# Optimization experiments

Hardware: AMD Instinct MI355X
Metric: run time of the kernel (lower is better)

The kernel has to match this reference:

```python
import jax, jax.numpy as jnp
import numpy as np

B, C = 2, 128
FMAP_HW = [(256, 256), (128, 128), (64, 64), (32, 32)]
N_ROIS = 4000
POOL = (7, 7)
N_ANCH = 300000
N_POS = 1000          # anchors with match > 0 (class 1)
N_NEG = 200000        # anchors with match == -1
SHEM_POOLSIZE = 20
N_CLASSES = 2


def setup_inputs() -> dict:
    key = jax.random.key(0)
    ks = jax.random.split(key, 10)
    inp = {}
    for l, (h, w) in enumerate(FMAP_HW):
        inp[f"fmap{l}"] = jax.random.normal(ks[l], (B, C, h, w), dtype=jnp.float32)
    # rois: normalized (y1, x1, y2, x2, batch_ix)
    ctr = jax.random.uniform(ks[4], (N_ROIS, 2))
    sz = jax.random.uniform(ks[5], (N_ROIS, 2), minval=0.02, maxval=0.5)
    lo = jnp.clip(ctr - sz / 2, 0.0, 1.0)
    hi = jnp.clip(ctr + sz / 2, 0.0, 1.0)
    bix = jax.random.randint(ks[6], (N_ROIS, 1), 0, B).astype(jnp.float32)
    inp["rois"] = jnp.concatenate([lo, hi, bix], axis=1)
    # fixed layout for static shapes: [pos | neg | neutral]
    am = np.zeros(N_ANCH, np.int32)
    am[:N_POS] = 1
    am[N_POS:N_POS + N_NEG] = -1
    inp["anchor_matches"] = jnp.asarray(am)
    inp["class_pred_logits"] = jax.random.normal(ks[7], (N_ANCH, N_CLASSES), dtype=jnp.float32)
    inp["pred_deltas"] = jax.random.normal(ks[8], (N_ANCH, 4), dtype=jnp.float32) * 0.1
    inp["target_deltas"] = jax.random.normal(ks[9], (N_ANCH, 4), dtype=jnp.float32) * 0.1
    return inp


def _roi_align_2d(fmap, boxes, batch_ix, pool):
    """Bilinear ROI align, one sample at each bin center.
    fmap: [B,C,H,W]; boxes: [N,4] in fmap pixel coords (y1,x1,y2,x2).
    Returns [N,C,ph,pw]."""
    Hc, Wc = fmap.shape[2], fmap.shape[3]
    ph, pw = pool
    y1, x1, y2, x2 = boxes[:, 0], boxes[:, 1], boxes[:, 2], boxes[:, 3]
    bh = (y2 - y1) / ph
    bw = (x2 - x1) / pw
    iy = jnp.arange(ph, dtype=jnp.float32) + 0.5
    ix = jnp.arange(pw, dtype=jnp.float32) + 0.5
    sy = jnp.clip(y1[:, None] + bh[:, None] * iy[None, :], 0.0, Hc - 1.0)  # [N,ph]
    sx = jnp.clip(x1[:, None] + bw[:, None] * ix[None, :], 0.0, Wc - 1.0)  # [N,pw]
    y0f = jnp.floor(sy)
    x0f = jnp.floor(sx)
    y0 = y0f.astype(jnp.int32)
    x0 = x0f.astype(jnp.int32)
    y1i = jnp.minimum(y0 + 1, Hc - 1)
    x1i = jnp.minimum(x0 + 1, Wc - 1)
    wy = (sy - y0f)[:, :, None, None]  # [N,ph,1,1]
    wx = (sx - x0f)[:, None, :, None]  # [N,1,pw,1]
    b = batch_ix[:, None, None]

    def gather(yy, xx):
        # yy [N,ph], xx [N,pw] -> [N,ph,pw,C]
        return fmap[b, :, yy[:, :, None], xx[:, None, :]]

    v00 = gather(y0, x0)
    v01 = gather(y0, x1i)
    v10 = gather(y1i, x0)
    v11 = gather(y1i, x1i)
    out = (v00 * (1 - wy) * (1 - wx) + v01 * (1 - wy) * wx
           + v10 * wy * (1 - wx) + v11 * wy * wx)
    return jnp.transpose(out, (0, 3, 1, 2))


def _forward(fmaps, rois, anchor_matches, class_pred_logits, pred_deltas, target_deltas):
    boxes = rois[:, :4]
    batch_ix = rois[:, 4].astype(jnp.int32)
    h = boxes[:, 2] - boxes[:, 0]
    w = boxes[:, 3] - boxes[:, 1]
    roi_level = jnp.clip(
        jnp.round(4.0 + jnp.log2(jnp.sqrt(h * w + 1e-12))).astype(jnp.int32), 0, 3)
    boxes_sg = jax.lax.stop_gradient(boxes)  # original detaches level_boxes
    pooled = jnp.zeros((N_ROIS, C, POOL[0], POOL[1]), fmaps[0].dtype)
    for lvl, f in enumerate(fmaps):
        He, We = f.shape[2], f.shape[3]
        lb = boxes_sg * jnp.array([He, We, He, We], jnp.float32)
        pl = _roi_align_2d(f, lb, batch_ix, POOL)
        mask = (roi_level == lvl).astype(pl.dtype)[:, None, None, None]
        pooled = pooled + mask * pl  # each roi hits exactly one level; order preserved

    # ---- class loss with SHEM (layout: [:N_POS] pos, [N_POS:N_POS+N_NEG] neg) ----
    pos_logits = class_pred_logits[:N_POS]
    pos_targets = anchor_matches[:N_POS].astype(jnp.int32)
    pos_logp = jax.nn.log_softmax(pos_logits, axis=1)
    pos_loss = -jnp.mean(jnp.take_along_axis(pos_logp, pos_targets[:, None], axis=1))

    neg_logits = class_pred_logits[N_POS:N_POS + N_NEG]
    neg_bg_prob = jax.nn.softmax(neg_logits, axis=1)[:, 0]
    negative_count = N_POS  # max(1, n_pos)
    pool_n = min(negative_count * SHEM_POOLSIZE, N_NEG)
    order = jnp.argsort(neg_bg_prob)          # ascending bg prob = hardest first
    pool_idx = order[:pool_n]
    perm = jax.random.permutation(jax.random.key(1), pool_n)
    neg_ix = pool_idx[perm[:negative_count]]  # stochastic draw from hard pool
    neg_loss = -jnp.mean(jax.nn.log_softmax(neg_logits[neg_ix], axis=1)[:, 0])
    class_loss = (pos_loss + neg_loss) / 2.0

    # ---- bbox smooth-L1 on positives (beta=1, mean reduction) ----
    diff = jnp.abs(pred_deltas[:N_POS] - target_deltas[:N_POS])
    sl1 = jnp.where(diff < 1.0, 0.5 * diff * diff, diff - 0.5)
    bbox_loss = jnp.mean(sl1)
    return pooled, class_loss, bbox_loss


def reference(fmap0, fmap1, fmap2, fmap3, rois, anchor_matches,
              class_pred_logits, pred_deltas, target_deltas):
    return _forward([fmap0, fmap1, fmap2, fmap3], rois, anchor_matches,
                    class_pred_logits, pred_deltas, target_deltas)
```

## Files before the change

kernel.cpp:

```cpp
#include <hip/hip_runtime.h>
#include <hip/hip_bf16.h>
#include <cstdint>

#define NROIS  4000
#define NCH    128
#define NBINS  49
#define N_POSA 1000
#define N_NEGA 200000
#define POOLN  20000
#define HBITS_A 13
#define ABINS  8192
#define PBINS  4096
#define SUBN   4096
#define NTRBLK 2720
#define NPREP  106
#define NRANKA 512
#define NRANKP 40
#define TPAD   136

#define L0OFF 0ull
#define L1OFF 16777216ull
#define L2OFF 20971520ull
#define L3OFF 22020096ull
#define TLELEMS 22282240ull

__device__ __forceinline__ uint32_t rotl32d(uint32_t v, int r) { return (v << r) | (v >> (32-r)); }

__device__ void tf2x32(uint32_t k0, uint32_t k1, uint32_t& x0, uint32_t& x1)
{
    const uint32_t ks2 = k0 ^ k1 ^ 0x1BD11BDAu;
    const int R0[4] = {13,15,26,6};
    const int R1[4] = {17,29,16,24};
    x0 += k0; x1 += k1;
#pragma unroll
    for (int r = 0; r < 4; ++r) { x0 += x1; x1 = rotl32d(x1, R0[r]); x1 ^= x0; }
    x0 += k1;  x1 += ks2 + 1u;
#pragma unroll
    for (int r = 0; r < 4; ++r) { x0 += x1; x1 = rotl32d(x1, R1[r]); x1 ^= x0; }
    x0 += ks2; x1 += k0 + 2u;
#pragma unroll
    for (int r = 0; r < 4; ++r) { x0 += x1; x1 = rotl32d(x1, R0[r]); x1 ^= x0; }
    x0 += k0;  x1 += k1 + 3u;
#pragma unroll
    for (int r = 0; r < 4; ++r) { x0 += x1; x1 = rotl32d(x1, R1[r]); x1 ^= x0; }
    x0 += k1;  x1 += ks2 + 4u;
#pragma unroll
    for (int r = 0; r < 4; ++r) { x0 += x1; x1 = rotl32d(x1, R0[r]); x1 ^= x0; }
    x0 += ks2; x1 += k0 + 5u;
}

__device__ __forceinline__ unsigned int monobits(float x) {
    unsigned int u = __float_as_uint(x);
    return (u & 0x80000000u) ? ~u : (u | 0x80000000u);
}

__device__ __forceinline__ unsigned short f2bf(float x) {
    union { __hip_bfloat16 h; unsigned short u; } c;
    c.h = __float2bfloat16(x);
    return c.u;
}

__global__ void k_zero(unsigned int* __restrict__ h)
{
    h[blockIdx.x*256 + threadIdx.x] = 0u;
}

__global__ __launch_bounds__(256) void k_trprep(
    const float* __restrict__ f0, const float* __restrict__ f1,
    const float* __restrict__ f2, const float* __restrict__ f3,
    __hip_bfloat16* __restrict__ tl,
    unsigned long long* __restrict__ T1, unsigned long long* __restrict__ T2,
    unsigned int* __restrict__ histA,
    unsigned int* __restrict__ histP1, unsigned int* __restrict__ histP2,
    const int* __restrict__ am, const float* __restrict__ logits,
    const float* __restrict__ pd, const float* __restrict__ td,
    float* __restrict__ prt, int ntr)
{
    __shared__ __align__(16) unsigned char smraw[32768];
    const int bid = blockIdx.x;
    const int t   = threadIdx.x;

    if (bid < ntr) {
        unsigned short* s = (unsigned short*)smraw;
        const int bz = bid / 1360;
        const int r  = bid - bz*1360;
        int lvl, tile;
        if      (r < 1024) { lvl = 0; tile = r; }
        else if (r < 1280) { lvl = 1; tile = r - 1024; }
        else if (r < 1344) { lvl = 2; tile = r - 1280; }
        else               { lvl = 3; tile = r - 1344; }
        const int HW = 65536 >> (2*lvl);
        const float* in = (lvl==0) ? f0 : (lvl==1) ? f1 : (lvl==2) ? f2 : f3;
        const size_t ooff = (lvl==0) ? L0OFF : (lvl==1) ? L1OFF : (lvl==2) ? L2OFF : L3OFF;
        const int hw0 = tile * 64;
        const float4* in4 = (const float4*)(in + (size_t)bz * 128 * HW);
        const int HW4 = HW >> 2;
        const int h4b = hw0 >> 2;
#pragma unroll
        for (int k = 0; k < 8; ++k) {
            const int idx = t + k*256;
            const int c   = idx >> 4;
            const int h4  = idx & 15;
            const float4 v = in4[(size_t)c * HW4 + h4b + h4];
            const int r0 = h4 * 4;
            const int cs = c ^ ((h4 & 7) << 3);
            s[(r0+0)*TPAD + cs] = f2bf(v.x);
            s[(r0+1)*TPAD + cs] = f2bf(v.y);
            s[(r0+2)*TPAD + cs] = f2bf(v.z);
            s[(r0+3)*TPAD + cs] = f2bf(v.w);
        }
        __syncthreads();
        uint4* out4 = (uint4*)(tl + ooff + (size_t)bz * (size_t)HW * 128
                                         + (size_t)hw0 * 128);
        const int rr = t >> 4;
        const int q  = t & 15;
        const int c8 = q * 8;
#pragma unroll
        for (int m = 0; m < 4; ++m) {
            const int row = rr + m*16;
            const int sw = ((row >> 2) & 7) << 3;
            out4[row*16 + q] = *(const uint4*)&s[row*TPAD + (c8 ^ sw)];
        }
        return;
    }

    const int pbid = bid - ntr;
    if (pbid < 40) {
        unsigned int* buf = (unsigned int*)smraw;
        unsigned int* lh1 = buf;
        unsigned int* lh2 = buf + PBINS;
        for (int b = t; b < 2*PBINS; b += 256) buf[b] = 0u;
        __syncthreads();
        const int i = pbid*256 + t;
        if (i < POOLN/2) {
            uint32_t a0 = 0u, a1 = 2u; tf2x32(0u, 1u, a0, a1);
            uint32_t b0 = 1u, b1 = 3u; tf2x32(0u, 1u, b0, b1);
            uint32_t c0 = 0u, c1 = 2u; tf2x32(a0, b0, c0, c1);
            uint32_t d0 = 1u, d1 = 3u; tf2x32(a0, b0, d0, d1);
            uint32_t x0 = (uint32_t)i, x1 = (uint32_t)(POOLN/2 + i);
            tf2x32(a1, b1, x0, x1);
            T1[i]           = ((unsigned long long)x0 << 32) | (unsigned)i;
            T1[POOLN/2 + i] = ((unsigned long long)x1 << 32) | (unsigned)(POOLN/2 + i);
            atomicAdd(&lh1[x0 >> 20], 1u);
            atomicAdd(&lh1[x1 >> 20], 1u);
            uint32_t y0 = (uint32_t)i, y1 = (uint32_t)(POOLN/2 + i);
            tf2x32(c1, d1, y0, y1);
            T2[i]           = ((unsigned long long)y0 << 32) | (unsigned)i;
            T2[POOLN/2 + i] = ((unsigned long long)y1 << 32) | (unsigned)(POOLN/2 + i);
            atomicAdd(&lh2[y0 >> 20], 1u);
            atomicAdd(&lh2[y1 >> 20], 1u);
        }
        __syncthreads();
        for (int b = t; b < PBINS; b += 256) {
            unsigned int v = lh1[b]; if (v) atomicAdd(&histP1[b], v);
            v = lh2[b];              if (v) atomicAdd(&histP2[b], v);
        }
        return;
    }
    if (pbid < 104) {
        unsigned int* buf = (unsigned int*)smraw;
        for (int b = t; b < ABINS; b += 256) buf[b] = 0u;
        __syncthreads();
        for (int i = (pbid-40)*256 + t; i < N_NEGA; i += 64*256) {
            const float l0 = logits[(size_t)(N_POSA+i)*2+0];
            const float l1 = logits[(size_t)(N_POSA+i)*2+1];
            atomicAdd(&buf[monobits(l0 - l1) >> (32-HBITS_A)], 1u);
        }
        __syncthreads();
        for (int b = t; b < ABINS; b += 256) {
            const unsigned int v = buf[b];
            if (v) atomicAdd(&histA[b], v);
        }
        return;
    }
    float* red = (float*)smraw;
    float s = 0.0f;
    if (pbid == 104) {
        for (int i = t; i < N_POSA; i += 256) {
            const int tgt = am[i];
            const float l0 = logits[(size_t)i*2+0], l1 = logits[(size_t)i*2+1];
            const float m = fmaxf(l0, l1);
            const float lse = logf(expf(l0-m) + expf(l1-m));
            const float lt = (tgt == 0) ? l0 : l1;
            s += (lt - m) - lse;
        }
    } else {
        for (int i = t; i < N_POSA*4; i += 256) {
            const float d = fabsf(pd[i] - td[i]);
            s += (d < 1.0f) ? 0.5f*d*d : d - 0.5f;
        }
    }
    red[t] = s;
    __syncthreads();
    for (int off = 128; off > 0; off >>= 1) {
        if (t < off) red[t] += red[t+off];
        __syncthreads();
    }
    if (t == 0) prt[pbid - 104] = red[0];
}

__device__ void scan_one256(const unsigned int* __restrict__ hist,
                            unsigned int* __restrict__ base,
                            unsigned int* __restrict__ basem,
                            int n, unsigned int* lds)
{
    const int t = threadIdx.x;
    const int chunk = n >> 8;
    unsigned int s = 0;
    for (int k = 0; k < chunk; ++k) s += hist[t*chunk + k];
    lds[t] = s;
    __syncthreads();
    for (int off = 1; off < 256; off <<= 1) {
        unsigned int v = (t >= off) ? lds[t-off] : 0u;
        __syncthreads();
        lds[t] += v;
        __syncthreads();
    }
    unsigned int run = (t == 0) ? 0u : lds[t-1];
    for (int k = 0; k < chunk; ++k) {
        base[t*chunk+k] = run; basem[t*chunk+k] = run;
        run += hist[t*chunk+k];
    }
    if (t == 255) { base[n] = run; basem[n] = run; }
    __syncthreads();
}

__device__ void scan_all(const unsigned int* histA, const unsigned int* histP1,
                         const unsigned int* histP2,
                         unsigned int* baseA,  unsigned int* baseAm,
                         unsigned int* baseP1, unsigned int* baseP1m,
                         unsigned int* baseP2, unsigned int* baseP2m,
                         unsigned int* sel, unsigned int* lds)
{
    scan_one256(histA, baseA, baseAm, ABINS, lds);
    scan_one256(histP1, baseP1, baseP1m, PBINS, lds);
    scan_one256(histP2, baseP2, baseP2m, PBINS, lds);
    const int t = threadIdx.x;
    const int chunk = ABINS >> 8;
    for (int k = 0; k < chunk; ++k) {
        const int bin = t*chunk + k;
        if (baseA[bin] < POOLN && baseA[bin] + histA[bin] >= POOLN)
            sel[0] = (unsigned int)bin;
    }
}

__global__ __launch_bounds__(256) void k_roiscan(
    const __hip_bfloat16* __restrict__ tl, const float* __restrict__ rois,
    float* __restrict__ out,
    const unsigned int* __restrict__ histA,
    const unsigned int* __restrict__ histP1, const unsigned int* __restrict__ histP2,
    unsigned int* __restrict__ baseA,  unsigned int* __restrict__ baseAm,
    unsigned int* __restrict__ baseP1, unsigned int* __restrict__ baseP1m,
    unsigned int* __restrict__ baseP2, unsigned int* __restrict__ baseP2m,
    unsigned int* __restrict__ sel, int nroi)
{
    __shared__ int   s_a[NBINS][4];
    __shared__ float s_w[NBINS][4];
    __shared__ float s_o[NCH * NBINS];
    const int n   = blockIdx.x;
    const int tid = threadIdx.x;

    if (n >= nroi) {
        scan_all(histA, histP1, histP2, baseA, baseAm, baseP1, baseP1m,
                 baseP2, baseP2m, sel, (unsigned int*)s_o);
        return;
    }

    const float ry1 = rois[n*5+0], rx1 = rois[n*5+1];
    const float ry2 = rois[n*5+2], rx2 = rois[n*5+3];
    const int   b   = (int)rois[n*5+4];
    const float h = ry2 - ry1, w = rx2 - rx1;
    const float lraw = rintf(4.0f + log2f(sqrtf(h*w + 1e-12f)));
    int lvl = (int)lraw; lvl = lvl < 0 ? 0 : (lvl > 3 ? 3 : lvl);
    const int H = 256 >> lvl;
    const size_t lbase = (lvl==0) ? L0OFF : (lvl==1) ? L1OFF : (lvl==2) ? L2OFF : L3OFF;
    const __hip_bfloat16* bp = tl + lbase + (size_t)b * (size_t)(H*H) * NCH;

    const float Hf  = (float)H;
    const float y1p = ry1*Hf, x1p = rx1*Hf, y2p = ry2*Hf, x2p = rx2*Hf;
    const float bh = (y2p - y1p) / 7.0f, bw = (x2p - x1p) / 7.0f;

    if (tid < NBINS) {
        const int py = tid / 7, px = tid % 7;
        float sy = y1p + bh*((float)py + 0.5f);
        float sx = x1p + bw*((float)px + 0.5f);
        sy = fminf(fmaxf(sy, 0.0f), Hf - 1.0f);
        sx = fminf(fmaxf(sx, 0.0f), Hf - 1.0f);
        const float y0f = floorf(sy), x0f = floorf(sx);
        const int y0 = (int)y0f, x0 = (int)x0f;
        const int y1i = min(y0+1, H-1), x1i = min(x0+1, H-1);
        const float wy = sy - y0f, wx = sx - x0f;
        s_a[tid][0] = y0 *H + x0;
        s_a[tid][1] = y0 *H + x1i;
        s_a[tid][2] = y1i*H + x0;
        s_a[tid][3] = y1i*H + x1i;
        const float omy = 1.0f - wy, omx = 1.0f - wx;
        s_w[tid][0] = omy*omx; s_w[tid][1] = omy*wx;
        s_w[tid][2] = wy *omx; s_w[tid][3] = wy *wx;
    }
    __syncthreads();

    const int c4 = tid & 31;
    const int bg = tid >> 5;
    for (int bin = bg; bin < NBINS; bin += 8) {
        float a0 = 0.f, a1 = 0.f, a2 = 0.f, a3 = 0.f;
#pragma unroll
        for (int tap = 0; tap < 4; ++tap) {
            const uint2 v = *(const uint2*)(bp + (size_t)s_a[bin][tap] * NCH + 4*c4);
            const float wgt = s_w[bin][tap];
            a0 += __uint_as_float(v.x << 16)         * wgt;
            a1 += __uint_as_float(v.x & 0xffff0000u) * wgt;
            a2 += __uint_as_float(v.y << 16)         * wgt;
            a3 += __uint_as_float(v.y & 0xffff0000u) * wgt;
        }
        s_o[(4*c4+0)*NBINS + bin] = a0;
        s_o[(4*c4+1)*NBINS + bin] = a1;
        s_o[(4*c4+2)*NBINS + bin] = a2;
        s_o[(4*c4+3)*NBINS + bin] = a3;
    }
    __syncthreads();

    float4* outn = (float4*)(out + (size_t)n * (NCH*NBINS));
    const float4* so4 = (const float4*)s_o;
    for (int t4 = tid; t4 < (NCH*NBINS)/4; t4 += 256)
        outn[t4] = so4[t4];
}

__global__ __launch_bounds__(256) void k_roi(
    const float* __restrict__ f0, const float* __restrict__ f1,
    const float* __restrict__ f2, const float* __restrict__ f3,
    const float* __restrict__ rois, float* __restrict__ out)
{
    __shared__ int   s_a[NBINS][4];
    __shared__ float s_w[NBINS][4];
    const int n   = blockIdx.x;
    const int tid = threadIdx.x;

    const float ry1 = rois[n*5+0], rx1 = rois[n*5+1];
    const float ry2 = rois[n*5+2], rx2 = rois[n*5+3];
    const int   b   = (int)rois[n*5+4];
    const float h = ry2 - ry1, w = rx2 - rx1;
    const float lraw = rintf(4.0f + log2f(sqrtf(h*w + 1e-12f)));
    int lvl = (int)lraw; lvl = lvl < 0 ? 0 : (lvl > 3 ? 3 : lvl);
    const int H = 256 >> lvl;
    const float* f = (lvl==0) ? f0 : (lvl==1) ? f1 : (lvl==2) ? f2 : f3;

    const float Hf  = (float)H;
    const float y1p = ry1*Hf, x1p = rx1*Hf, y2p = ry2*Hf, x2p = rx2*Hf;
    const float bh = (y2p - y1p) / 7.0f, bw = (x2p - x1p) / 7.0f;

    if (tid < NBINS) {
        const int py = tid / 7, px = tid % 7;
        float sy = y1p + bh*((float)py + 0.5f);
        float sx = x1p + bw*((float)px + 0.5f);
        sy = fminf(fmaxf(sy, 0.0f), Hf - 1.0f);
        sx = fminf(fmaxf(sx, 0.0f), Hf - 1.0f);
        const float y0f = floorf(sy), x0f = floorf(sx);
        const int y0 = (int)y0f, x0 = (int)x0f;
        const int y1i = min(y0+1, H-1), x1i = min(x0+1, H-1);
        const float wy = sy - y0f, wx = sx - x0f;
        s_a[tid][0] = y0 *H + x0;
        s_a[tid][1] = y0 *H + x1i;
        s_a[tid][2] = y1i*H + x0;
        s_a[tid][3] = y1i*H + x1i;
        const float omy = 1.0f - wy, omx = 1.0f - wx;
        s_w[tid][0] = omy*omx; s_w[tid][1] = omy*wx;
        s_w[tid][2] = wy *omx; s_w[tid][3] = wy *wx;
    }
    __syncthreads();

    const int hw = H*H;
    const float* basep = f + (size_t)b * NCH * hw;
    float* outn = out + (size_t)n * (NCH*NBINS);
    for (int t = tid; t < NCH*NBINS; t += 256) {
        const int c   = t / NBINS;
        const int bin = t - c*NBINS;
        const float* p = basep + (size_t)c * hw;
        outn[t] = p[s_a[bin][0]]*s_w[bin][0] + p[s_a[bin][1]]*s_w[bin][1]
                + p[s_a[bin][2]]*s_w[bin][2] + p[s_a[bin][3]]*s_w[bin][3];
    }
}

__global__ __launch_bounds__(256) void k_scatter(
    const float* __restrict__ logits,
    const unsigned long long* __restrict__ T1, const unsigned long long* __restrict__ T2,
    unsigned long long* __restrict__ A,
    unsigned long long* __restrict__ P1, unsigned long long* __restrict__ P2,
    unsigned int* __restrict__ baseAm, unsigned int* __restrict__ baseP1m,
    unsigned int* __restrict__ baseP2m, const unsigned int* __restrict__ sel)
{
    __shared__ unsigned int lh[ABINS];
    const int bid = blockIdx.x;
    const int t   = threadIdx.x;
    if (bid < 64) {
        for (int b = t; b < ABINS; b += 256) lh[b] = 0u;
        __syncthreads();
        const unsigned int selv = sel[0];
        const int start = bid * (N_NEGA/64);
        const int end   = start + (N_NEGA/64);
        for (int i = start + t; i < end; i += 256) {
            const float l0 = logits[(size_t)(N_POSA+i)*2+0];
            const float l1 = logits[(size_t)(N_POSA+i)*2+1];
            const unsigned int bin = monobits(l0 - l1) >> (32-HBITS_A);
            if (bin <= selv) atomicAdd(&lh[bin], 1u);
        }
        __syncthreads();
        for (int b = t; b < ABINS; b += 256) {
            const unsigned int cnt = lh[b];
            if (cnt) lh[b] = atomicAdd(&baseAm[b], cnt);
        }
        __syncthreads();
        for (int i = start + t; i < end; i += 256) {
            const float l0 = logits[(size_t)(N_POSA+i)*2+0];
            const float l1 = logits[(size_t)(N_POSA+i)*2+1];
            const unsigned int bits = monobits(l0 - l1);
            const unsigned int bin = bits >> (32-HBITS_A);
            if (bin <= selv) {
                const unsigned int pos = atomicAdd(&lh[bin], 1u);
                A[pos] = ((unsigned long long)bits << 32) | (unsigned)i;
            }
        }
        return;
    }
    const int i = (bid - 64)*256 + t;
    if (i < POOLN) {
        const unsigned long long k1 = T1[i];
        const unsigned int p1 = atomicAdd(&baseP1m[(unsigned)(k1 >> 52)], 1u);
        P1[p1] = k1;
        const unsigned long long k2 = T2[i];
        const unsigned int p2 = atomicAdd(&baseP2m[(unsigned)(k2 >> 52)], 1u);
        P2[p2] = k2;
    }
}

__global__ __launch_bounds__(1024) void k_rank(
    const unsigned long long* __restrict__ A,
    const unsigned long long* __restrict__ P1, const unsigned long long* __restrict__ P2,
    const unsigned int* __restrict__ baseA,
    const unsigned int* __restrict__ baseP1, const unsigned int* __restrict__ baseP2,
    const unsigned int* __restrict__ sel,
    unsigned int* __restrict__ As, unsigned int* __restrict__ P1s,
    unsigned int* __restrict__ P2s)
{
    __shared__ unsigned long long g[SUBN];
    __shared__ unsigned int h2[SUBN];
    __shared__ unsigned int h2b[SUBN];
    const int bid = blockIdx.x;
    const int t   = threadIdx.x;
    if (bid < NRANKA) {
        const unsigned int selv = sel[0];
        for (unsigned int bin = (unsigned)bid; bin <= selv; bin += NRANKA) {
            const int base = (int)baseA[bin];
            const int cnt  = (int)baseA[bin+1] - base;
            if (cnt <= 0) continue;
            if (cnt == 1) {
                if (t == 0) As[base] = (unsigned)(A[base] & 0xffffffffu);
                continue;
            }
            if (cnt <= SUBN) {
                for (int b = t; b < SUBN; b += 1024) h2[b] = 0u;
                __syncthreads();
                for (int k = t; k < cnt; k += 1024) {
                    const unsigned int sub = ((unsigned)(A[base+k] >> 32) >> 7) & (SUBN-1);
                    atomicAdd(&h2[sub], 1u);
                }
                __syncthreads();
                unsigned int c0 = h2[4*t+0], c1 = h2[4*t+1],
                             c2 = h2[4*t+2], c3 = h2[4*t+3];
                h2b[t] = c0 + c1 + c2 + c3;
                __syncthreads();
                for (int off = 1; off < 1024; off <<= 1) {
                    const unsigned int v = (t >= off) ? h2b[t-off] : 0u;
                    __syncthreads();
                    h2b[t] += v;
                    __syncthreads();
                }
                unsigned int run = (t == 0) ? 0u : h2b[t-1];
                __syncthreads();
                h2[4*t+0] = run; h2b[4*t+0] = run; run += c0;
                h2[4*t+1] = run; h2b[4*t+1] = run; run += c1;
                h2[4*t+2] = run; h2b[4*t+2] = run; run += c2;
                h2[4*t+3] = run; h2b[4*t+3] = run; run += c3;
                __syncthreads();
                for (int k = t; k < cnt; k += 1024) {
                    const unsigned long long key = A[base+k];
                    const unsigned int sub = ((unsigned)(key >> 32) >> 7) & (SUBN-1);
                    const unsigned int p = atomicAdd(&h2[sub], 1u);
                    g[p] = key;
                }
                __syncthreads();
                for (int p = t; p < cnt; p += 1024) {
                    const unsigned long long key = g[p];
                    const unsigned int sub = ((unsigned)(key >> 32) >> 7) & (SUBN-1);
                    const int b0 = (int)h2b[sub], e0 = (int)h2[sub];
                    int r = b0;
                    for (int q = b0; q < e0; ++q) r += (g[q] < key) ? 1 : 0;
                    As[base + r] = (unsigned)(key & 0xffffffffu);
                }
                __syncthreads();
            } else {
                for (int k = t; k < cnt; k += 1024) {
                    const unsigned long long key = A[base+k];
                    int rank = 0;
                    for (int j = 0; j < cnt; ++j) rank += (A[base+j] < key) ? 1 : 0;
                    As[base + rank] = (unsigned)(key & 0xffffffffu);
                }
            }
        }
        return;
    }
    const int gg = (bid - NRANKA)*1024 + t;
    if (gg < POOLN) {
        const unsigned long long key = P1[gg];
        const unsigned int bin = (unsigned)(key >> 52);
        const int b0 = (int)baseP1[bin], b1 = (int)baseP1[bin+1];
        int rank = 0;
        for (int j = b0; j < b1; ++j) rank += (P1[j] < key) ? 1 : 0;
        P1s[b0 + rank] = (unsigned)(key & 0xffffffffu);
    } else if (gg < 2*POOLN) {
        const int e = gg - POOLN;
        const unsigned long long key = P2[e];
        const unsigned int bin = (unsigned)(key >> 52);
        const int b0 = (int)baseP2[bin], b1 = (int)baseP2[bin+1];
        int rank = 0;
        for (int j = b0; j < b1; ++j) rank += (P2[j] < key) ? 1 : 0;
        P2s[b0 + rank] = (unsigned)(key & 0xffffffffu);
    }
}

__global__ __launch_bounds__(256) void k_final(
    const float* __restrict__ logits, const unsigned int* __restrict__ As,
    const unsigned int* __restrict__ P1s, const unsigned int* __restrict__ P2s,
    const float* __restrict__ partial, float* __restrict__ out2)
{
    __shared__ float red[256];
    const int t = threadIdx.x;
    float s = 0.0f;
    for (int j = t; j < N_POSA; j += 256) {
        const unsigned int i2 = P2s[j];
        const unsigned int r  = P1s[i2];
        const unsigned int i  = As[r];
        const float l0 = logits[(size_t)(N_POSA+i)*2+0];
        const float l1 = logits[(size_t)(N_POSA+i)*2+1];
        const float m = fmaxf(l0, l1);
        s += (l0 - m) - logf(expf(l0-m) + expf(l1-m));
    }
    red[t] = s;
    __syncthreads();
    for (int off = 128; off > 0; off >>= 1) {
        if (t < off) red[t] += red[t+off];
        __syncthreads();
    }
    if (t == 0) {
        const float neg_loss = -red[0] / (float)N_POSA;
        const float pos_loss = -partial[0] / (float)N_POSA;
        out2[0] = 0.5f * (pos_loss + neg_loss);
        out2[1] = partial[1] / (float)(N_POSA*4);
    }
}

extern "C" void kernel_launch(void* const* d_in, const int* in_sizes, int n_in,
                              void* d_out, int out_size, void* d_ws, size_t ws_size,
                              hipStream_t stream)
{
    const float* f0     = (const float*)d_in[0];
    const float* f1     = (const float*)d_in[1];
    const float* f2     = (const float*)d_in[2];
    const float* f3     = (const float*)d_in[3];
    const float* rois   = (const float*)d_in[4];
    const int*   am     = (const int*)  d_in[5];
    const float* logits = (const float*)d_in[6];
    const float* pd     = (const float*)d_in[7];
    const float* td     = (const float*)d_in[8];
    float* out = (float*)d_out;

    char* ws = (char*)d_ws;
    unsigned long long* A      = (unsigned long long*)(ws);
    unsigned long long* T1     = (unsigned long long*)(ws +  262144);
    unsigned long long* T2     = (unsigned long long*)(ws +  422144);
    unsigned long long* P1     = (unsigned long long*)(ws +  582144);
    unsigned long long* P2     = (unsigned long long*)(ws +  742144);
    unsigned int*       histA  = (unsigned int*)      (ws +  902144);
    unsigned int*       histP1 = (unsigned int*)      (ws +  934912);
    unsigned int*       histP2 = (unsigned int*)      (ws +  951296);
    unsigned int*       baseA  = (unsigned int*)      (ws +  967680);
    unsigned int*       baseAm = (unsigned int*)      (ws + 1000512);
    unsigned int*       baseP1 = (unsigned int*)      (ws + 1033344);
    unsigned int*       baseP1m= (unsigned int*)      (ws + 1049792);
    unsigned int*       baseP2 = (unsigned int*)      (ws + 1066240);
    unsigned int*       baseP2m= (unsigned int*)      (ws + 1082688);
    unsigned int*       sel    = (unsigned int*)      (ws + 1099136);
    float*              prt    = (float*)             (ws + 1099200);
    __hip_bfloat16*     tl     = (__hip_bfloat16*)    (ws + 1099264);
    unsigned int*       As     = (unsigned int*)T1;
    unsigned int*       P1s    = (unsigned int*)T2;
    unsigned int*       P2s    = (unsigned int*)((char*)T2 + 80000);
    const size_t NEED = 1099264ull + TLELEMS * 2ull;
    const bool use_cl = (ws_size >= NEED);

    k_zero<<<64, 256, 0, stream>>>(histA);

    if (use_cl) {
        k_trprep<<<NTRBLK + NPREP, 256, 0, stream>>>(f0, f1, f2, f3, tl,
                                                     T1, T2, histA, histP1, histP2,
                                                     am, logits, pd, td, prt, NTRBLK);
        k_roiscan<<<NROIS + 1, 256, 0, stream>>>(tl, rois, out,
                                                 histA, histP1, histP2,
                                                 baseA, baseAm, baseP1, baseP1m,
                                                 baseP2, baseP2m, sel, NROIS);
    } else {
        k_trprep<<<NPREP, 256, 0, stream>>>(f0, f1, f2, f3, tl,
                                            T1, T2, histA, histP1, histP2,
                                            am, logits, pd, td, prt, 0);
        k_roi<<<NROIS, 256, 0, stream>>>(f0, f1, f2, f3, rois, out);
        k_roiscan<<<1, 256, 0, stream>>>(tl, rois, out,
                                         histA, histP1, histP2,
                                         baseA, baseAm, baseP1, baseP1m,
                                         baseP2, baseP2m, sel, 0);
    }

    k_scatter<<<64 + (POOLN+255)/256, 256, 0, stream>>>(logits, T1, T2, A, P1, P2,
                                                        baseAm, baseP1m, baseP2m, sel);

    k_rank<<<NRANKA + NRANKP, 1024, 0, stream>>>(A, P1, P2, baseA, baseP1, baseP2,
                                                 sel, As, P1s, P2s);

    k_final<<<1, 256, 0, stream>>>(logits, As, P1s, P2s, prt,
                                   out + (size_t)NROIS*NCH*NBINS);
}
```

Measured before the change: 102.8 us.

## Interleave transpose and ROI-align blocks with the sort stages across launches

```diff
diff --git a/kernel.cpp b/kernel.cpp
--- a/kernel.cpp
+++ b/kernel.cpp
@@ -12,10 +12,11 @@
 #define ABINS  8192
 #define PBINS  4096
 #define SUBN   4096
-#define NTRBLK 2720
+#define NTR_H  1360
 #define NPREP  106
+#define NSCAT  143
 #define NRANKA 512
-#define NRANKP 40
+#define NRANKP 157
 #define TPAD   136
 
 #define L0OFF 0ull
@@ -65,7 +66,124 @@
     h[blockIdx.x*256 + threadIdx.x] = 0u;
 }
 
-__global__ __launch_bounds__(256) void k_trprep(
+__device__ void do_transpose(int trid, const float* __restrict__ f0,
+                             const float* __restrict__ f1, const float* __restrict__ f2,
+                             const float* __restrict__ f3,
+                             __hip_bfloat16* __restrict__ tl, unsigned char* smraw)
+{
+    unsigned short* s = (unsigned short*)smraw;
+    const int t  = threadIdx.x;
+    const int bz = trid / NTR_H;
+    const int r  = trid - bz*NTR_H;
+    int lvl, tile;
+    if      (r < 1024) { lvl = 0; tile = r; }
+    else if (r < 1280) { lvl = 1; tile = r - 1024; }
+    else if (r < 1344) { lvl = 2; tile = r - 1280; }
+    else               { lvl = 3; tile = r - 1344; }
+    const int HW = 65536 >> (2*lvl);
+    const float* in = (lvl==0) ? f0 : (lvl==1) ? f1 : (lvl==2) ? f2 : f3;
+    const size_t ooff = (lvl==0) ? L0OFF : (lvl==1) ? L1OFF : (lvl==2) ? L2OFF : L3OFF;
+    const int hw0 = tile * 64;
+    const float4* in4 = (const float4*)(in + (size_t)bz * 128 * HW);
+    const int HW4 = HW >> 2;
+    const int h4b = hw0 >> 2;
+#pragma unroll
+    for (int k = 0; k < 8; ++k) {
+        const int idx = t + k*256;
+        const int c   = idx >> 4;
+        const int h4  = idx & 15;
+        const float4 v = in4[(size_t)c * HW4 + h4b + h4];
+        const int r0 = h4 * 4;
+        const int cs = c ^ ((h4 & 7) << 3);
+        s[(r0+0)*TPAD + cs] = f2bf(v.x);
+        s[(r0+1)*TPAD + cs] = f2bf(v.y);
+        s[(r0+2)*TPAD + cs] = f2bf(v.z);
+        s[(r0+3)*TPAD + cs] = f2bf(v.w);
+    }
+    __syncthreads();
+    uint4* out4 = (uint4*)(tl + ooff + (size_t)bz * (size_t)HW * 128
+                                     + (size_t)hw0 * 128);
+    const int rr = t >> 4;
+    const int q  = t & 15;
+    const int c8 = q * 8;
+#pragma unroll
+    for (int m = 0; m < 4; ++m) {
+        const int row = rr + m*16;
+        const int sw = ((row >> 2) & 7) << 3;
+        out4[row*16 + q] = *(const uint4*)&s[row*TPAD + (c8 ^ sw)];
+    }
+}
+
+__device__ void do_roi(int n, const __hip_bfloat16* __restrict__ tl,
+                       const float* __restrict__ rois, float* __restrict__ out,
+                       unsigned char* smraw)
+{
+    int   (*s_a)[4] = (int(*)[4])smraw;
+    float (*s_w)[4] = (float(*)[4])(smraw + 784);
+    float* s_o      = (float*)(smraw + 1568);
+    const int tid = threadIdx.x;
+
+    const float ry1 = rois[n*5+0], rx1 = rois[n*5+1];
+    const float ry2 = rois[n*5+2], rx2 = rois[n*5+3];
+    const int   b   = (int)rois[n*5+4];
+    const float h = ry2 - ry1, w = rx2 - rx1;
+    const float lraw = rintf(4.0f + log2f(sqrtf(h*w + 1e-12f)));
+    int lvl = (int)lraw; lvl = lvl < 0 ? 0 : (lvl > 3 ? 3 : lvl);
+    const int H = 256 >> lvl;
+    const size_t lbase = (lvl==0) ? L0OFF : (lvl==1) ? L1OFF : (lvl==2) ? L2OFF : L3OFF;
+    const __hip_bfloat16* bp = tl + lbase + (size_t)b * (size_t)(H*H) * NCH;
+
+    const float Hf  = (float)H;
+    const float y1p = ry1*Hf, x1p = rx1*Hf, y2p = ry2*Hf, x2p = rx2*Hf;
+    const float bh = (y2p - y1p) / 7.0f, bw = (x2p - x1p) / 7.0f;
+
+    if (tid < NBINS) {
+        const int py = tid / 7, px = tid % 7;
+        float sy = y1p + bh*((float)py + 0.5f);
+        float sx = x1p + bw*((float)px + 0.5f);
+        sy = fminf(fmaxf(sy, 0.0f), Hf - 1.0f);
+        sx = fminf(fmaxf(sx, 0.0f), Hf - 1.0f);
+        const float y0f = floorf(sy), x0f = floorf(sx);
+        const int y0 = (int)y0f, x0 = (int)x0f;
+        const int y1i = min(y0+1, H-1), x1i = min(x0+1, H-1);
+        const float wy = sy - y0f, wx = sx - x0f;
+        s_a[tid][0] = y0 *H + x0;
+        s_a[tid][1] = y0 *H + x1i;
+        s_a[tid][2] = y1i*H + x0;
+        s_a[tid][3] = y1i*H + x1i;
+        const float omy = 1.0f - wy, omx = 1.0f - wx;
+        s_w[tid][0] = omy*omx; s_w[tid][1] = omy*wx;
+        s_w[tid][2] = wy *omx; s_w[tid][3] = wy *wx;
+    }
+    __syncthreads();
+
+    const int c4 = tid & 31;
+    const int bg = tid >> 5;
+    for (int bin = bg; bin < NBINS; bin += 8) {
+        float a0 = 0.f, a1 = 0.f, a2 = 0.f, a3 = 0.f;
+#pragma unroll
+        for (int tap = 0; tap < 4; ++tap) {
+            const uint2 v = *(const uint2*)(bp + (size_t)s_a[bin][tap] * NCH + 4*c4);
+            const float wgt = s_w[bin][tap];
+            a0 += __uint_as_float(v.x << 16)         * wgt;
+            a1 += __uint_as_float(v.x & 0xffff0000u) * wgt;
+            a2 += __uint_as_float(v.y << 16)         * wgt;
+            a3 += __uint_as_float(v.y & 0xffff0000u) * wgt;
+        }
+        s_o[(4*c4+0)*NBINS + bin] = a0;
+        s_o[(4*c4+1)*NBINS + bin] = a1;
+        s_o[(4*c4+2)*NBINS + bin] = a2;
+        s_o[(4*c4+3)*NBINS + bin] = a3;
+    }
+    __syncthreads();
+
+    float4* outn = (float4*)(out + (size_t)n * (NCH*NBINS));
+    const float4* so4 = (const float4*)s_o;
+    for (int t4 = tid; t4 < (NCH*NBINS)/4; t4 += 256)
+        outn[t4] = so4[t4];
+}
+
+__global__ __launch_bounds__(256) void k_stage1(
     const float* __restrict__ f0, const float* __restrict__ f1,
     const float* __restrict__ f2, const float* __restrict__ f3,
     __hip_bfloat16* __restrict__ tl,
@@ -80,49 +198,7 @@
     const int bid = blockIdx.x;
     const int t   = threadIdx.x;
 
-    if (bid < ntr) {
-        unsigned short* s = (unsigned short*)smraw;
-        const int bz = bid / 1360;
-        const int r  = bid - bz*1360;
-        int lvl, tile;
-        if      (r < 1024) { lvl = 0; tile = r; }
-        else if (r < 1280) { lvl = 1; tile = r - 1024; }
-        else if (r < 1344) { lvl = 2; tile = r - 1280; }
-        else               { lvl = 3; tile = r - 1344; }
-        const int HW = 65536 >> (2*lvl);
-        const float* in = (lvl==0) ? f0 : (lvl==1) ? f1 : (lvl==2) ? f2 : f3;
-        const size_t ooff = (lvl==0) ? L0OFF : (lvl==1) ? L1OFF : (lvl==2) ? L2OFF : L3OFF;
-        const int hw0 = tile * 64;
-        const float4* in4 = (const float4*)(in + (size_t)bz * 128 * HW);
-        const int HW4 = HW >> 2;
-        const int h4b = hw0 >> 2;
-#pragma unroll
-        for (int k = 0; k < 8; ++k) {
-            const int idx = t + k*256;
-            const int c   = idx >> 4;
-            const int h4  = idx & 15;
-            const float4 v = in4[(size_t)c * HW4 + h4b + h4];
-            const int r0 = h4 * 4;
-            const int cs = c ^ ((h4 & 7) << 3);
-            s[(r0+0)*TPAD + cs] = f2bf(v.x);
-            s[(r0+1)*TPAD + cs] = f2bf(v.y);
-            s[(r0+2)*TPAD + cs] = f2bf(v.z);
-            s[(r0+3)*TPAD + cs] = f2bf(v.w);
-        }
-        __syncthreads();
-        uint4* out4 = (uint4*)(tl + ooff + (size_t)bz * (size_t)HW * 128
-                                         + (size_t)hw0 * 128);
-        const int rr = t >> 4;
-        const int q  = t & 15;
-        const int c8 = q * 8;
-#pragma unroll
-        for (int m = 0; m < 4; ++m) {
-            const int row = rr + m*16;
-            const int sw = ((row >> 2) & 7) << 3;
-            out4[row*16 + q] = *(const uint4*)&s[row*TPAD + (c8 ^ sw)];
-        }
-        return;
-    }
+    if (bid < ntr) { do_transpose(bid, f0, f1, f2, f3, tl, smraw); return; }
 
     const int pbid = bid - ntr;
     if (pbid < 40) {
@@ -225,13 +301,22 @@
     __syncthreads();
 }
 
-__device__ void scan_all(const unsigned int* histA, const unsigned int* histP1,
-                         const unsigned int* histP2,
-                         unsigned int* baseA,  unsigned int* baseAm,
-                         unsigned int* baseP1, unsigned int* baseP1m,
-                         unsigned int* baseP2, unsigned int* baseP2m,
-                         unsigned int* sel, unsigned int* lds)
-{
+__global__ __launch_bounds__(256) void k_stage2(
+    const float* __restrict__ f0, const float* __restrict__ f1,
+    const float* __restrict__ f2, const float* __restrict__ f3,
+    __hip_bfloat16* __restrict__ tl,
+    const unsigned int* __restrict__ histA,
+    const unsigned int* __restrict__ histP1, const unsigned int* __restrict__ histP2,
+    unsigned int* __restrict__ baseA,  unsigned int* __restrict__ baseAm,
+    unsigned int* __restrict__ baseP1, unsigned int* __restrict__ baseP1m,
+    unsigned int* __restrict__ baseP2, unsigned int* __restrict__ baseP2m,
+    unsigned int* __restrict__ sel, int ntr)
+{
+    __shared__ __align__(16) unsigned char smraw[32768];
+    const int bid = blockIdx.x;
+    if (bid < ntr) { do_transpose(bid + NTR_H, f0, f1, f2, f3, tl, smraw); return; }
+
+    unsigned int* lds = (unsigned int*)smraw;
     scan_one256(histA, baseA, baseAm, ABINS, lds);
     scan_one256(histP1, baseP1, baseP1m, PBINS, lds);
     scan_one256(histP2, baseP2, baseP2m, PBINS, lds);
@@ -244,27 +329,188 @@
     }
 }
 
-__global__ __launch_bounds__(256) void k_roiscan(
+__global__ __launch_bounds__(256) void k_stage3(
+    const __hip_bfloat16* __restrict__ tl, const float* __restrict__ rois,
+    float* __restrict__ out, const float* __restrict__ logits,
+    const unsigned long long* __restrict__ T1, const unsigned long long* __restrict__ T2,
+    unsigned long long* __restrict__ A,
+    unsigned long long* __restrict__ P1, unsigned long long* __restrict__ P2,
+    unsigned int* __restrict__ baseAm, unsigned int* __restrict__ baseP1m,
+    unsigned int* __restrict__ baseP2m, const unsigned int* __restrict__ sel,
+    int rcnt)
+{
+    __shared__ __align__(16) unsigned char smraw[32768];
+    const int bid = blockIdx.x;
+    const int t   = threadIdx.x;
+    if (bid < rcnt) { do_roi(bid, tl, rois, out, smraw); return; }
+
+    const int sbid = bid - rcnt;
+    if (sbid < 64) {
+        unsigned int* lh = (unsigned int*)smraw;
+        for (int b = t; b < ABINS; b += 256) lh[b] = 0u;
+        __syncthreads();
+        const unsigned int selv = sel[0];
+        const int start = sbid * (N_NEGA/64);
+        const int end   = start + (N_NEGA/64);
+        for (int i = start + t; i < end; i += 256) {
+            const float l0 = logits[(size_t)(N_POSA+i)*2+0];
+            const float l1 = logits[(size_t)(N_POSA+i)*2+1];
+            const unsigned int bin = monobits(l0 - l1) >> (32-HBITS_A);
+            if (bin <= selv) atomicAdd(&lh[bin], 1u);
+        }
+        __syncthreads();
+        for (int b = t; b < ABINS; b += 256) {
+            const unsigned int cnt = lh[b];
+            if (cnt) lh[b] = atomicAdd(&baseAm[b], cnt);
+        }
+        __syncthreads();
+        for (int i = start + t; i < end; i += 256) {
+            const float l0 = logits[(size_t)(N_POSA+i)*2+0];
+            const float l1 = logits[(size_t)(N_POSA+i)*2+1];
+            const unsigned int bits = monobits(l0 - l1);
+            const unsigned int bin = bits >> (32-HBITS_A);
+            if (bin <= selv) {
+                const unsigned int pos = atomicAdd(&lh[bin], 1u);
+                A[pos] = ((unsigned long long)bits << 32) | (unsigned)i;
+            }
+        }
+        return;
+    }
+    const int i = (sbid - 64)*256 + t;
+    if (i < POOLN) {
+        const unsigned long long k1 = T1[i];
+        const unsigned int p1 = atomicAdd(&baseP1m[(unsigned)(k1 >> 52)], 1u);
+        P1[p1] = k1;
+        const unsigned long long k2 = T2[i];
+        const unsigned int p2 = atomicAdd(&baseP2m[(unsigned)(k2 >> 52)], 1u);
+        P2[p2] = k2;
+    }
+}
+
+__global__ __launch_bounds__(256) void k_stage4(
     const __hip_bfloat16* __restrict__ tl, const float* __restrict__ rois,
     float* __restrict__ out,
-    const unsigned int* __restrict__ histA,
-    const unsigned int* __restrict__ histP1, const unsigned int* __restrict__ histP2,
-    unsigned int* __restrict__ baseA,  unsigned int* __restrict__ baseAm,
-    unsigned int* __restrict__ baseP1, unsigned int* __restrict__ baseP1m,
-    unsigned int* __restrict__ baseP2, unsigned int* __restrict__ baseP2m,
-    unsigned int* __restrict__ sel, int nroi)
+    const unsigned long long* __restrict__ A,
+    const unsigned long long* __restrict__ P1, const unsigned long long* __restrict__ P2,
+    const unsigned int* __restrict__ baseA,
+    const unsigned int* __restrict__ baseP1, const unsigned int* __restrict__ baseP2,
+    const unsigned int* __restrict__ sel,
+    unsigned int* __restrict__ As, unsigned int* __restrict__ P1s,
+    unsigned int* __restrict__ P2s, int rcnt)
+{
+    __shared__ __align__(16) unsigned char smraw[32768];
+    const int bid = blockIdx.x;
+    const int t   = threadIdx.x;
+    if (bid < rcnt) { do_roi(2000 + bid, tl, rois, out, smraw); return; }
+
+    const int sbid = bid - rcnt;
+    if (sbid < NRANKA) {
+        unsigned int*   gkey = (unsigned int*)smraw;
+        unsigned short* gsub = (unsigned short*)(smraw + 16384);
+        unsigned int*   h2p  = (unsigned int*)(smraw + 24576);
+        unsigned int*   st   = (unsigned int*)(smraw + 16384);
+        const unsigned int selv = sel[0];
+        for (unsigned int bin = (unsigned)sbid; bin <= selv; bin += NRANKA) {
+            const int base = (int)baseA[bin];
+            const int cnt  = (int)baseA[bin+1] - base;
+            if (cnt <= 0) continue;
+            if (cnt == 1) {
+                if (t == 0) As[base] = (unsigned)(A[base] & 0xffffffffu);
+                continue;
+            }
+            if (cnt <= SUBN) {
+                for (int b = t; b < SUBN/2; b += 256) h2p[b] = 0u;
+                __syncthreads();
+                for (int k = t; k < cnt; k += 256) {
+                    const unsigned int sub =
+                        ((unsigned)(A[base+k] >> 32) >> 7) & (SUBN-1);
+                    atomicAdd(&h2p[sub >> 1], 1u << ((sub & 1) << 4));
+                }
+                __syncthreads();
+                unsigned int tmp[8];
+                unsigned int s = 0;
+                for (int w = 0; w < 8; ++w) {
+                    const unsigned int v = h2p[t*8 + w];
+                    tmp[w] = v;
+                    s += (v & 0xFFFFu) + (v >> 16);
+                }
+                st[t] = s;
+                __syncthreads();
+                for (int off = 1; off < 256; off <<= 1) {
+                    const unsigned int v = (t >= off) ? st[t-off] : 0u;
+                    __syncthreads();
+                    st[t] += v;
+                    __syncthreads();
+                }
+                unsigned int run = (t == 0) ? 0u : st[t-1];
+                __syncthreads();
+                for (int w = 0; w < 8; ++w) {
+                    const unsigned int v = tmp[w];
+                    const unsigned int lo = run; run += (v & 0xFFFFu);
+                    const unsigned int hi = run; run += (v >> 16);
+                    h2p[t*8 + w] = lo | (hi << 16);
+                }
+                __syncthreads();
+                for (int k = t; k < cnt; k += 256) {
+                    const unsigned long long key = A[base+k];
+                    const unsigned int bits = (unsigned)(key >> 32);
+                    const unsigned int sub  = (bits >> 7) & (SUBN-1);
+                    const unsigned int sh   = (sub & 1) << 4;
+                    const unsigned int old  = atomicAdd(&h2p[sub >> 1], 1u << sh);
+                    const unsigned int pos  = (old >> sh) & 0xFFFFu;
+                    gkey[pos] = ((bits & 0x7Fu) << 18) | (unsigned)(key & 0xffffffffu);
+                    gsub[pos] = (unsigned short)sub;
+                }
+                __syncthreads();
+                for (int p = t; p < cnt; p += 256) {
+                    const unsigned int k25 = gkey[p];
+                    const unsigned short sb = gsub[p];
+                    int b0 = p; while (b0 > 0 && gsub[b0-1] == sb) --b0;
+                    int e0 = p; while (e0+1 < cnt && gsub[e0+1] == sb) ++e0;
+                    int r = b0;
+                    for (int q = b0; q <= e0; ++q) r += (gkey[q] < k25) ? 1 : 0;
+                    As[base + r] = k25 & 0x3FFFFu;
+                }
+                __syncthreads();
+            } else {
+                for (int k = t; k < cnt; k += 256) {
+                    const unsigned long long key = A[base+k];
+                    int rank = 0;
+                    for (int j = 0; j < cnt; ++j) rank += (A[base+j] < key) ? 1 : 0;
+                    As[base + rank] = (unsigned)(key & 0xffffffffu);
+                }
+            }
+        }
+        return;
+    }
+    const int g = (sbid - NRANKA)*256 + t;
+    if (g < POOLN) {
+        const unsigned long long key = P1[g];
+        const unsigned int bin = (unsigned)(key >> 52);
+        const int b0 = (int)baseP1[bin], b1 = (int)baseP1[bin+1];
+        int rank = 0;
+        for (int j = b0; j < b1; ++j) rank += (P1[j] < key) ? 1 : 0;
+        P1s[b0 + rank] = (unsigned)(key & 0xffffffffu);
+    } else if (g < 2*POOLN) {
+        const int e = g - POOLN;
+        const unsigned long long key = P2[e];
+        const unsigned int bin = (unsigned)(key >> 52);
+        const int b0 = (int)baseP2[bin], b1 = (int)baseP2[bin+1];
+        int rank = 0;
+        for (int j = b0; j < b1; ++j) rank += (P2[j] < key) ? 1 : 0;
+        P2s[b0 + rank] = (unsigned)(key & 0xffffffffu);
+    }
+}
+
+__global__ __launch_bounds__(256) void k_roi(
+    const float* __restrict__ f0, const float* __restrict__ f1,
+    const float* __restrict__ f2, const float* __restrict__ f3,
+    const float* __restrict__ rois, float* __restrict__ out)
 {
     __shared__ int   s_a[NBINS][4];
     __shared__ float s_w[NBINS][4];
-    __shared__ float s_o[NCH * NBINS];
     const int n   = blockIdx.x;
     const int tid = threadIdx.x;
-
-    if (n >= nroi) {
-        scan_all(histA, histP1, histP2, baseA, baseAm, baseP1, baseP1m,
-                 baseP2, baseP2m, sel, (unsigned int*)s_o);
-        return;
-    }
 
     const float ry1 = rois[n*5+0], rx1 = rois[n*5+1];
     const float ry2 = rois[n*5+2], rx2 = rois[n*5+3];
@@ -273,8 +519,7 @@
     const float lraw = rintf(4.0f + log2f(sqrtf(h*w + 1e-12f)));
     int lvl = (int)lraw; lvl = lvl < 0 ? 0 : (lvl > 3 ? 3 : lvl);
     const int H = 256 >> lvl;
-    const size_t lbase = (lvl==0) ? L0OFF : (lvl==1) ? L1OFF : (lvl==2) ? L2OFF : L3OFF;
-    const __hip_bfloat16* bp = tl + lbase + (size_t)b * (size_t)(H*H) * NCH;
+    const float* f = (lvl==0) ? f0 : (lvl==1) ? f1 : (lvl==2) ? f2 : f3;
 
     const float Hf  = (float)H;
     const float y1p = ry1*Hf, x1p = rx1*Hf, y2p = ry2*Hf, x2p = rx2*Hf;
@@ -300,75 +545,6 @@
     }
     __syncthreads();
 
-    const int c4 = tid & 31;
-    const int bg = tid >> 5;
-    for (int bin = bg; bin < NBINS; bin += 8) {
-        float a0 = 0.f, a1 = 0.f, a2 = 0.f, a3 = 0.f;
-#pragma unroll
-        for (int tap = 0; tap < 4; ++tap) {
-            const uint2 v = *(const uint2*)(bp + (size_t)s_a[bin][tap] * NCH + 4*c4);
-            const float wgt = s_w[bin][tap];
-            a0 += __uint_as_float(v.x << 16)         * wgt;
-            a1 += __uint_as_float(v.x & 0xffff0000u) * wgt;
-            a2 += __uint_as_float(v.y << 16)         * wgt;
-            a3 += __uint_as_float(v.y & 0xffff0000u) * wgt;
-        }
-        s_o[(4*c4+0)*NBINS + bin] = a0;
-        s_o[(4*c4+1)*NBINS + bin] = a1;
-        s_o[(4*c4+2)*NBINS + bin] = a2;
-        s_o[(4*c4+3)*NBINS + bin] = a3;
-    }
-    __syncthreads();
-
-    float4* outn = (float4*)(out + (size_t)n * (NCH*NBINS));
-    const float4* so4 = (const float4*)s_o;
-    for (int t4 = tid; t4 < (NCH*NBINS)/4; t4 += 256)
-        outn[t4] = so4[t4];
-}
-
-__global__ __launch_bounds__(256) void k_roi(
-    const float* __restrict__ f0, const float* __restrict__ f1,
-    const float* __restrict__ f2, const float* __restrict__ f3,
-    const float* __restrict__ rois, float* __restrict__ out)
-{
-    __shared__ int   s_a[NBINS][4];
-    __shared__ float s_w[NBINS][4];
-    const int n   = blockIdx.x;
-    const int tid = threadIdx.x;
-
-    const float ry1 = rois[n*5+0], rx1 = rois[n*5+1];
-    const float ry2 = rois[n*5+2], rx2 = rois[n*5+3];
-    const int   b   = (int)rois[n*5+4];
-    const float h = ry2 - ry1, w = rx2 - rx1;
-    const float lraw = rintf(4.0f + log2f(sqrtf(h*w + 1e-12f)));
-    int lvl = (int)lraw; lvl = lvl < 0 ? 0 : (lvl > 3 ? 3 : lvl);
-    const int H = 256 >> lvl;
-    const float* f = (lvl==0) ? f0 : (lvl==1) ? f1 : (lvl==2) ? f2 : f3;
-
-    const float Hf  = (float)H;
-    const float y1p = ry1*Hf, x1p = rx1*Hf, y2p = ry2*Hf, x2p = rx2*Hf;
-    const float bh = (y2p - y1p) / 7.0f, bw = (x2p - x1p) / 7.0f;
-
-    if (tid < NBINS) {
-        const int py = tid / 7, px = tid % 7;
-        float sy = y1p + bh*((float)py + 0.5f);
-        float sx = x1p + bw*((float)px + 0.5f);
-        sy = fminf(fmaxf(sy, 0.0f), Hf - 1.0f);
-        sx = fminf(fmaxf(sx, 0.0f), Hf - 1.0f);
-        const float y0f = floorf(sy), x0f = floorf(sx);
-        const int y0 = (int)y0f, x0 = (int)x0f;
-        const int y1i = min(y0+1, H-1), x1i = min(x0+1, H-1);
-        const float wy = sy - y0f, wx = sx - x0f;
-        s_a[tid][0] = y0 *H + x0;
-        s_a[tid][1] = y0 *H + x1i;
-        s_a[tid][2] = y1i*H + x0;
-        s_a[tid][3] = y1i*H + x1i;
-        const float omy = 1.0f - wy, omx = 1.0f - wx;
-        s_w[tid][0] = omy*omx; s_w[tid][1] = omy*wx;
-        s_w[tid][2] = wy *omx; s_w[tid][3] = wy *wx;
-    }
-    __syncthreads();
-
     const int hw = H*H;
     const float* basep = f + (size_t)b * NCH * hw;
     float* outn = out + (size_t)n * (NCH*NBINS);
@@ -378,153 +554,6 @@
         const float* p = basep + (size_t)c * hw;
         outn[t] = p[s_a[bin][0]]*s_w[bin][0] + p[s_a[bin][1]]*s_w[bin][1]
                 + p[s_a[bin][2]]*s_w[bin][2] + p[s_a[bin][3]]*s_w[bin][3];
-    }
-}
-
-__global__ __launch_bounds__(256) void k_scatter(
-    const float* __restrict__ logits,
-    const unsigned long long* __restrict__ T1, const unsigned long long* __restrict__ T2,
-    unsigned long long* __restrict__ A,
-    unsigned long long* __restrict__ P1, unsigned long long* __restrict__ P2,
-    unsigned int* __restrict__ baseAm, unsigned int* __restrict__ baseP1m,
-    unsigned int* __restrict__ baseP2m, const unsigned int* __restrict__ sel)
-{
-    __shared__ unsigned int lh[ABINS];
-    const int bid = blockIdx.x;
-    const int t   = threadIdx.x;
-    if (bid < 64) {
-        for (int b = t; b < ABINS; b += 256) lh[b] = 0u;
-        __syncthreads();
-        const unsigned int selv = sel[0];
-        const int start = bid * (N_NEGA/64);
-        const int end   = start + (N_NEGA/64);
-        for (int i = start + t; i < end; i += 256) {
-            const float l0 = logits[(size_t)(N_POSA+i)*2+0];
-            const float l1 = logits[(size_t)(N_POSA+i)*2+1];
-            const unsigned int bin = monobits(l0 - l1) >> (32-HBITS_A);
-            if (bin <= selv) atomicAdd(&lh[bin], 1u);
-        }
-        __syncthreads();
-        for (int b = t; b < ABINS; b += 256) {
-            const unsigned int cnt = lh[b];
-            if (cnt) lh[b] = atomicAdd(&baseAm[b], cnt);
-        }
-        __syncthreads();
-        for (int i = start + t; i < end; i += 256) {
-            const float l0 = logits[(size_t)(N_POSA+i)*2+0];
-            const float l1 = logits[(size_t)(N_POSA+i)*2+1];
-            const unsigned int bits = monobits(l0 - l1);
-            const unsigned int bin = bits >> (32-HBITS_A);
-            if (bin <= selv) {
-                const unsigned int pos = atomicAdd(&lh[bin], 1u);
-                A[pos] = ((unsigned long long)bits << 32) | (unsigned)i;
-            }
-        }
-        return;
-    }
-    const int i = (bid - 64)*256 + t;
-    if (i < POOLN) {
-        const unsigned long long k1 = T1[i];
-        const unsigned int p1 = atomicAdd(&baseP1m[(unsigned)(k1 >> 52)], 1u);
-        P1[p1] = k1;
-        const unsigned long long k2 = T2[i];
-        const unsigned int p2 = atomicAdd(&baseP2m[(unsigned)(k2 >> 52)], 1u);
-        P2[p2] = k2;
-    }
-}
-
-__global__ __launch_bounds__(1024) void k_rank(
-    const unsigned long long* __restrict__ A,
-    const unsigned long long* __restrict__ P1, const unsigned long long* __restrict__ P2,
-    const unsigned int* __restrict__ baseA,
-    const unsigned int* __restrict__ baseP1, const unsigned int* __restrict__ baseP2,
-    const unsigned int* __restrict__ sel,
-    unsigned int* __restrict__ As, unsigned int* __restrict__ P1s,
-    unsigned int* __restrict__ P2s)
-{
-    __shared__ unsigned long long g[SUBN];
-    __shared__ unsigned int h2[SUBN];
-    __shared__ unsigned int h2b[SUBN];
-    const int bid = blockIdx.x;
-    const int t   = threadIdx.x;
-    if (bid < NRANKA) {
-        const unsigned int selv = sel[0];
-        for (unsigned int bin = (unsigned)bid; bin <= selv; bin += NRANKA) {
-            const int base = (int)baseA[bin];
-            const int cnt  = (int)baseA[bin+1] - base;
-            if (cnt <= 0) continue;
-            if (cnt == 1) {
-                if (t == 0) As[base] = (unsigned)(A[base] & 0xffffffffu);
-                continue;
-            }
-            if (cnt <= SUBN) {
-                for (int b = t; b < SUBN; b += 1024) h2[b] = 0u;
-                __syncthreads();
-                for (int k = t; k < cnt; k += 1024) {
-                    const unsigned int sub = ((unsigned)(A[base+k] >> 32) >> 7) & (SUBN-1);
-                    atomicAdd(&h2[sub], 1u);
-                }
-                __syncthreads();
-                unsigned int c0 = h2[4*t+0], c1 = h2[4*t+1],
-                             c2 = h2[4*t+2], c3 = h2[4*t+3];
-                h2b[t] = c0 + c1 + c2 + c3;
-                __syncthreads();
-                for (int off = 1; off < 1024; off <<= 1) {
-                    const unsigned int v = (t >= off) ? h2b[t-off] : 0u;
-                    __syncthreads();
-                    h2b[t] += v;
-                    __syncthreads();
-                }
-                unsigned int run = (t == 0) ? 0u : h2b[t-1];
-                __syncthreads();
-                h2[4*t+0] = run; h2b[4*t+0] = run; run += c0;
-                h2[4*t+1] = run; h2b[4*t+1] = run; run += c1;
-                h2[4*t+2] = run; h2b[4*t+2] = run; run += c2;
-                h2[4*t+3] = run; h2b[4*t+3] = run; run += c3;
-                __syncthreads();
-                for (int k = t; k < cnt; k += 1024) {
-                    const unsigned long long key = A[base+k];
-                    const unsigned int sub = ((unsigned)(key >> 32) >> 7) & (SUBN-1);
-                    const unsigned int p = atomicAdd(&h2[sub], 1u);
-                    g[p] = key;
-                }
-                __syncthreads();
-                for (int p = t; p < cnt; p += 1024) {
-                    const unsigned long long key = g[p];
-                    const unsigned int sub = ((unsigned)(key >> 32) >> 7) & (SUBN-1);
-                    const int b0 = (int)h2b[sub], e0 = (int)h2[sub];
-                    int r = b0;
-                    for (int q = b0; q < e0; ++q) r += (g[q] < key) ? 1 : 0;
-                    As[base + r] = (unsigned)(key & 0xffffffffu);
-                }
-                __syncthreads();
-            } else {
-                for (int k = t; k < cnt; k += 1024) {
-                    const unsigned long long key = A[base+k];
-                    int rank = 0;
-                    for (int j = 0; j < cnt; ++j) rank += (A[base+j] < key) ? 1 : 0;
-                    As[base + rank] = (unsigned)(key & 0xffffffffu);
-                }
-            }
-        }
-        return;
-    }
-    const int gg = (bid - NRANKA)*1024 + t;
-    if (gg < POOLN) {
-        const unsigned long long key = P1[gg];
-        const unsigned int bin = (unsigned)(key >> 52);
-        const int b0 = (int)baseP1[bin], b1 = (int)baseP1[bin+1];
-        int rank = 0;
-        for (int j = b0; j < b1; ++j) rank += (P1[j] < key) ? 1 : 0;
-        P1s[b0 + rank] = (unsigned)(key & 0xffffffffu);
-    } else if (gg < 2*POOLN) {
-        const int e = gg - POOLN;
-        const unsigned long long key = P2[e];
-        const unsigned int bin = (unsigned)(key >> 52);
-        const int b0 = (int)baseP2[bin], b1 = (int)baseP2[bin+1];
-        int rank = 0;
-        for (int j = b0; j < b1; ++j) rank += (P2[j] < key) ? 1 : 0;
-        P2s[b0 + rank] = (unsigned)(key & 0xffffffffu);
     }
 }
 
@@ -597,33 +626,31 @@
     unsigned int*       P2s    = (unsigned int*)((char*)T2 + 80000);
     const size_t NEED = 1099264ull + TLELEMS * 2ull;
     const bool use_cl = (ws_size >= NEED);
+    const int ntr  = use_cl ? NTR_H : 0;
+    const int rcnt = use_cl ? 2000 : 0;
 
     k_zero<<<64, 256, 0, stream>>>(histA);
 
-    if (use_cl) {
-        k_trprep<<<NTRBLK + NPREP, 256, 0, stream>>>(f0, f1, f2, f3, tl,
-                                                     T1, T2, histA, histP1, histP2,
-                                                     am, logits, pd, td, prt, NTRBLK);
-        k_roiscan<<<NROIS + 1, 256, 0, stream>>>(tl, rois, out,
-                                                 histA, histP1, histP2,
-                                                 baseA, baseAm, baseP1, baseP1m,
-                                                 baseP2, baseP2m, sel, NROIS);
-    } else {
-        k_trprep<<<NPREP, 256, 0, stream>>>(f0, f1, f2, f3, tl,
-                                            T1, T2, histA, histP1, histP2,
-                                            am, logits, pd, td, prt, 0);
+    k_stage1<<<ntr + NPREP, 256, 0, stream>>>(f0, f1, f2, f3, tl,
+                                              T1, T2, histA, histP1, histP2,
+                                              am, logits, pd, td, prt, ntr);
+
+    k_stage2<<<ntr + 1, 256, 0, stream>>>(f0, f1, f2, f3, tl,
+                                          histA, histP1, histP2,
+                                          baseA, baseAm, baseP1, baseP1m,
+                                          baseP2, baseP2m, sel, ntr);
+
+    if (!use_cl)
         k_roi<<<NROIS, 256, 0, stream>>>(f0, f1, f2, f3, rois, out);
-        k_roiscan<<<1, 256, 0, stream>>>(tl, rois, out,
-                                         histA, histP1, histP2,
-                                         baseA, baseAm, baseP1, baseP1m,
-                                         baseP2, baseP2m, sel, 0);
-    }
-
-    k_scatter<<<64 + (POOLN+255)/256, 256, 0, stream>>>(logits, T1, T2, A, P1, P2,
-                                                        baseAm, baseP1m, baseP2m, sel);
-
-    k_rank<<<NRANKA + NRANKP, 1024, 0, stream>>>(A, P1, P2, baseA, baseP1, baseP2,
-                                                 sel, As, P1s, P2s);
+
+    k_stage3<<<rcnt + NSCAT, 256, 0, stream>>>(tl, rois, out, logits,
+                                               T1, T2, A, P1, P2,
+                                               baseAm, baseP1m, baseP2m, sel, rcnt);
+
+    k_stage4<<<rcnt + NRANKA + NRANKP, 256, 0, stream>>>(tl, rois, out,
+                                                         A, P1, P2,
+                                                         baseA, baseP1, baseP2,
+                                                         sel, As, P1s, P2s, rcnt);
 
     k_final<<<1, 256, 0, stream>>>(logits, As, P1s, P2s, prt,
                                    out + (size_t)NROIS*NCH*NBINS);
```

Result: slower. 120.5 us (+17.2%).
